# Kernel tuning notes

Hardware: AMD Instinct MI355X
Metric: run time of the kernel (lower is better)

The kernel has to match this reference:

```python
import jax, jax.numpy as jnp
import numpy as np

B, S, XDIM, YDIM = 64, 1024, 256, 128


def setup_inputs() -> dict:
    key = jax.random.key(0)
    ks = jax.random.split(key, 7)
    q = jax.random.normal(ks[0], (B, S, XDIM), dtype=jnp.float32)
    # Linear weights in torch layout [out, in]; biases [out]
    sc = 1.0 / np.sqrt(XDIM)
    Wq = jax.random.normal(ks[1], (YDIM, XDIM), dtype=jnp.float32) * sc
    Wk = jax.random.normal(ks[2], (YDIM, XDIM), dtype=jnp.float32) * sc
    Wv = jax.random.normal(ks[3], (YDIM, XDIM), dtype=jnp.float32) * sc
    bq = jax.random.normal(ks[4], (YDIM,), dtype=jnp.float32) * sc
    bk = jax.random.normal(ks[5], (YDIM,), dtype=jnp.float32) * sc
    bv = jax.random.normal(ks[6], (YDIM,), dtype=jnp.float32) * sc
    return {"q": q, "Wq": Wq, "bq": bq, "Wk": Wk, "bk": bk, "Wv": Wv, "bv": bv}


def reference(q, Wq, bq, Wk, bk, Wv, bv):
    # Q, K, V projections: [B, S, YDIM]
    Q = jnp.einsum('bsx,yx->bsy', q, Wq) + bq
    K = jnp.einsum('bsx,yx->bsy', q, Wk) + bk
    V = jnp.einsum('bsx,yx->bsy', q, Wv) + bv
    scale = jnp.float32(np.sqrt(YDIM))
    # scores [B, S_q, S_k]; softmax over the QUERY axis (dim=-2), non-standard
    scores = jnp.einsum('bqd,bkd->bqk', Q, K) / scale
    attn = jax.nn.softmax(scores, axis=-2)
    out = jnp.einsum('bqk,bkd->bqd', attn, V)  # [B, S, YDIM]
    # flat=True: max over dim=-2 -> [B, YDIM]
    return jnp.max(out, axis=-2)
```

## Files before the change

kernel.cpp:

```cpp
#include <hip/hip_runtime.h>

typedef __bf16 bf16;
typedef __attribute__((ext_vector_type(8))) __bf16 bf16x8;
typedef __attribute__((ext_vector_type(4))) __bf16 bf16x4;
typedef __attribute__((ext_vector_type(4))) float  f32x4;

static __device__ __forceinline__ f32x4 mfma16(bf16x8 a, bf16x8 b, f32x4 c) {
  return __builtin_amdgcn_mfma_f32_16x16x32_bf16(a, b, c, 0, 0, 0);
}
static __device__ __forceinline__ float fexp2(float x) {
  return __builtin_amdgcn_exp2f(x);
}
static __device__ __forceinline__ float flog2(float x) {
  return __builtin_amdgcn_logf(x);
}

#define EXP_C1 (1.4426950408889634f / 11.313708498984760f)

typedef const __attribute__((address_space(1))) unsigned int gas_u32;
typedef __attribute__((address_space(3))) unsigned int las_u32;
#define GLDS16(gp, lp) __builtin_amdgcn_global_load_lds((gas_u32*)(gp), (las_u32*)(lp), 16, 0, 0)

#define WAITN0() __asm__ volatile("s_waitcnt vmcnt(0)" ::: "memory")


__global__ __launch_bounds__(256) void k_prep(
    const float* __restrict__ Wq, const float* __restrict__ Wk,
    const float* __restrict__ Wv, bf16* __restrict__ Wc, float* __restrict__ out)
{
  int id = blockIdx.x * 256 + threadIdx.x;
  if (id < 8192) out[id] = -__builtin_inff();
  int proj = id >> 12, r = id & 4095;
  int g = r >> 7, n = r & 127;
  const float* W = proj == 0 ? Wq : proj == 1 ? Wk : Wv;
  const float sc = (proj == 0) ? EXP_C1 : 1.0f;
  const float4* src = (const float4*)(W + n * 256 + g * 8);
  float4 a = src[0], b = src[1];
  bf16x8 o = { (bf16)(a.x * sc), (bf16)(a.y * sc), (bf16)(a.z * sc), (bf16)(a.w * sc),
               (bf16)(b.x * sc), (bf16)(b.y * sc), (bf16)(b.z * sc), (bf16)(b.w * sc) };
  *(bf16x8*)(Wc + (size_t)proj * 32768 + g * 1024 + n * 8) = o;
}

__global__ __launch_bounds__(256, 4) void k_qkv(
    const float* __restrict__ q, const bf16* __restrict__ Wc,
    const float* __restrict__ bq, const float* __restrict__ bk, const float* __restrict__ bv,
    bf16* __restrict__ Qb, bf16* __restrict__ Kb, bf16* __restrict__ VT)
{
  __shared__ bf16 Al[32 * 520];

  const int tid = threadIdx.x, lane = tid & 63, wave = tid >> 6;
  const int ln = lane & 15, quad = lane >> 4;
  const int wc = wave;
  const int m0 = blockIdx.x * 64;

  {
    const float* src = q + (size_t)m0 * 256;
    for (int it = 0; it < 16; ++it) {
      int f = it * 1024 + tid * 4;
      int r = f >> 8, c = f & 255;
      float4 v = *(const float4*)(src + f);
      bf16x4 o = { (bf16)v.x, (bf16)v.y, (bf16)v.z, (bf16)v.w };
      *(bf16x4*)&Al[(c >> 3) * 520 + r * 8 + (c & 7)] = o;
    }
  }
  __syncthreads();

  const int b = m0 >> 10, st = (m0 & 1023) >> 7, s_off = m0 & 64;
  const size_t tbase = ((size_t)b * 8 + st) * 16384;

  for (int p = 0; p < 3; ++p) {
    const bf16* W = Wc + (size_t)p * 32768;
    const float* bias = p == 0 ? bq : p == 1 ? bk : bv;
    if (p < 2) {
      f32x4 acc[2][4] = {};
      for (int kk = 0; kk < 8; ++kk) {
        int g = kk * 4 + quad;
        bf16x8 ax[4], bw[2];
        for (int t = 0; t < 4; ++t)
          ax[t] = *(const bf16x8*)&Al[g * 520 + (t * 16 + ln) * 8];
        for (int t = 0; t < 2; ++t)
          bw[t] = *(const bf16x8*)(W + g * 1024 + (wc * 32 + t * 16 + ln) * 8);
        for (int i = 0; i < 2; ++i)
          for (int j = 0; j < 4; ++j)
            acc[i][j] = mfma16(bw[i], ax[j], acc[i][j]);
      }
      bf16* dst = (p == 0 ? Qb : Kb) + tbase;
      for (int i = 0; i < 2; ++i) {
        float4 b4 = *(const float4*)&bias[wc * 32 + i * 16 + quad * 4];
        if (p == 0) { b4.x *= EXP_C1; b4.y *= EXP_C1; b4.z *= EXP_C1; b4.w *= EXP_C1; }
        int gd = wc * 4 + i * 2 + (quad >> 1);
        int e0 = (quad & 1) * 4;
        for (int j = 0; j < 4; ++j) {
          int s = s_off + j * 16 + ln;
          bf16x4 o = { (bf16)(acc[i][j][0] + b4.x), (bf16)(acc[i][j][1] + b4.y),
                       (bf16)(acc[i][j][2] + b4.z), (bf16)(acc[i][j][3] + b4.w) };
          *(bf16x4*)&dst[(size_t)gd * 1024 + (size_t)s * 8 + e0] = o;
        }
      }
    } else {
      f32x4 acc[4][2] = {};
      for (int kk = 0; kk < 8; ++kk) {
        int g = kk * 4 + quad;
        bf16x8 ax[4], bw[2];
        for (int t = 0; t < 4; ++t)
          ax[t] = *(const bf16x8*)&Al[g * 520 + (t * 16 + ln) * 8];
        for (int t = 0; t < 2; ++t)
          bw[t] = *(const bf16x8*)(W + g * 1024 + (wc * 32 + t * 16 + ln) * 8);
        for (int i = 0; i < 4; ++i)
          for (int j = 0; j < 2; ++j)
            acc[i][j] = mfma16(ax[i], bw[j], acc[i][j]);
      }
      bf16* dst = VT + tbase;
      for (int j = 0; j < 2; ++j) {
        int d = wc * 32 + j * 16 + ln;
        float bb = bias[d];
        for (int i = 0; i < 4; ++i) {
          int s0 = s_off + i * 16 + quad * 4;
          int G  = (s0 >> 5) * 4 + ((s0 & 15) >> 2);
          int e0 = (s0 & 16) >> 2;
          bf16x4 o = { (bf16)(acc[i][j][0] + bb), (bf16)(acc[i][j][1] + bb),
                       (bf16)(acc[i][j][2] + bb), (bf16)(acc[i][j][3] + bb) };
          *(bf16x4*)&dst[(size_t)G * 1024 + (size_t)d * 8 + e0] = o;
        }
      }
    }
  }
}

__global__ __launch_bounds__(256, 2) void k_stats(
    const bf16* __restrict__ Qb, const bf16* __restrict__ Kb, float* __restrict__ nlg)
{
  __shared__ char Qbuf[2][32768];
  const int b = blockIdx.x, kt = blockIdx.y;
  const int tid = threadIdx.x, lane = tid & 63, wave = tid >> 6;
  const int ln = lane & 15, quad = lane >> 4;

  const bf16* ktile = Kb + ((size_t)b * 8 + kt) * 16384;
  bf16x8 ak[2][4];
  for (int i = 0; i < 2; ++i)
    for (int kk = 0; kk < 4; ++kk)
      ak[i][kk] = *(const bf16x8*)(ktile + (kk * 4 + quad) * 1024 + (wave * 32 + i * 16 + ln) * 8);

  const char* qb_b = (const char*)(Qb + (size_t)b * 8 * 16384);
  for (int c = 0; c < 8; ++c)
    GLDS16(qb_b + (wave * 8 + c) * 1024 + lane * 16, &Qbuf[0][(wave * 8 + c) * 1024]);

  f32x4 csum[2] = {};
  for (int qt = 0; qt < 8; ++qt) {
    WAITN0();
    __syncthreads();
    if (qt < 7)
      for (int c = 0; c < 8; ++c)
        GLDS16(qb_b + (size_t)(qt + 1) * 32768 + (wave * 8 + c) * 1024 + lane * 16,
               &Qbuf[(qt + 1) & 1][(wave * 8 + c) * 1024]);
    const char* Ql = Qbuf[qt & 1];
    for (int jq = 0; jq < 8; ++jq) {
      f32x4 s0 = {}, s1 = {};
      __builtin_amdgcn_s_setprio(1);
      for (int kk = 0; kk < 4; ++kk) {
        bf16x8 bqf = *(const bf16x8*)(Ql + ((kk * 4 + quad) * 2 + (jq >> 2)) * 1024
                                         + ((jq * 16 + ln) & 63) * 16);
        s0 = mfma16(ak[0][kk], bqf, s0);
        s1 = mfma16(ak[1][kk], bqf, s1);
      }
      __builtin_amdgcn_s_setprio(0);
      for (int rr = 0; rr < 4; ++rr) {
        csum[0][rr] += fexp2(s0[rr]);
        csum[1][rr] += fexp2(s1[rr]);
      }
    }
  }
  for (int i = 0; i < 2; ++i)
    for (int rr = 0; rr < 4; ++rr) {
      float v = csum[i][rr];
      v += __shfl_xor(v, 1, 64); v += __shfl_xor(v, 2, 64);
      v += __shfl_xor(v, 4, 64); v += __shfl_xor(v, 8, 64);
      csum[i][rr] = v;
    }
  if (ln == 0) {
    float* dst = nlg + (size_t)b * 1024 + kt * 128 + wave * 32 + quad * 4;
    for (int i = 0; i < 2; ++i)
      for (int rr = 0; rr < 4; ++rr)
        dst[i * 16 + rr] = -flog2(csum[i][rr]);
  }
}

__global__ __launch_bounds__(256, 2) void k_attn(
    const bf16* __restrict__ Qb, const bf16* __restrict__ Kb, const bf16* __restrict__ VT,
    const float* __restrict__ nlg, float* __restrict__ out)
{
  __shared__ char bufK[2][16384];
  __shared__ char bufV[2][16384];
  __shared__ float nll[1024];
  __shared__ float redm[4][128];

  const int b = blockIdx.x, qt = blockIdx.y;
  const int tid = threadIdx.x, lane = tid & 63, wave = tid >> 6;
  const int ln = lane & 15, quad = lane >> 4;

  *(float4*)&nll[tid * 4] = *(const float4*)(nlg + (size_t)b * 1024 + tid * 4);

  const bf16* qtile = Qb + ((size_t)b * 8 + qt) * 16384;
  bf16x8 bq_[2][4];
  for (int j = 0; j < 2; ++j)
    for (int kk = 0; kk < 4; ++kk)
      bq_[j][kk] = *(const bf16x8*)(qtile + (kk * 4 + quad) * 1024 + (wave * 32 + j * 16 + ln) * 8);

  const char* kb_b = (const char*)(Kb + (size_t)b * 8 * 16384);
  const char* vt_b = (const char*)(VT + (size_t)b * 8 * 16384);

#define K_DMA(t) do {                                                            \
    const char* ksrc = kb_b + (size_t)((t) >> 1) * 32768 + ((t) & 1) * 1024;     \
    char* dk = bufK[(t) & 1];                                                    \
    for (int c = 0; c < 4; ++c) {                                                \
      int ch = wave * 4 + c;                                                     \
      GLDS16(ksrc + ch * 2048 + lane * 16, dk + ch * 1024);                      \
    }                                                                            \
  } while (0)
#define V_DMA(t) do {                                                            \
    const char* vsrc = vt_b + (size_t)((t) >> 1) * 32768 + ((t) & 1) * 16384;    \
    char* dv = bufV[(t) & 1];                                                    \
    for (int c = 0; c < 4; ++c) {                                                \
      int ch = wave * 4 + c;                                                     \
      GLDS16(vsrc + (ch >> 1) * 2048 + (ch & 1) * 1024 + lane * 16,              \
             dv + ch * 1024);                                                    \
    }                                                                            \
  } while (0)

#define QK(tt, SN) do {                                                          \
    const char* Kl = bufK[(tt) & 1];                                             \
    _Pragma("unroll")                                                            \
    for (int i = 0; i < 4; ++i) {                                                \
      float4 L4 = *(float4*)&nll[(tt) * 64 + i * 16 + quad * 4];                 \
      f32x4 ini = { L4.x, L4.y, L4.z, L4.w };                                    \
      SN[i][0] = ini; SN[i][1] = ini;                                            \
    }                                                                            \
    __builtin_amdgcn_s_setprio(1);                                               \
    _Pragma("unroll")                                                            \
    for (int kk = 0; kk < 4; ++kk) {                                             \
      bf16x8 ak[4];                                                              \
      _Pragma("unroll")                                                          \
      for (int i = 0; i < 4; ++i)                                                \
        ak[i] = *(const bf16x8*)(Kl + (kk * 4 + quad) * 1024 + (i * 16 + ln) * 16); \
      _Pragma("unroll")                                                          \
      for (int i = 0; i < 4; ++i) {                                              \
        SN[i][0] = mfma16(ak[i], bq_[0][kk], SN[i][0]);                          \
        SN[i][1] = mfma16(ak[i], bq_[1][kk], SN[i][1]);                          \
      }                                                                          \
    }                                                                            \
    __builtin_amdgcn_s_setprio(0);                                               \
  } while (0)

#define EXPPV(tt, SC) do {                                                       \
    const char* Vl = bufV[(tt) & 1];                                             \
    _Pragma("unroll")                                                            \
    for (int s = 0; s < 2; ++s) {                                                \
      f32x4 lo0 = SC[2 * s][0], hi0 = SC[2 * s + 1][0];                          \
      f32x4 lo1 = SC[2 * s][1], hi1 = SC[2 * s + 1][1];                          \
      bf16x8 pf0 = bf16x8{                                                       \
        (bf16)fexp2(lo0[0]), (bf16)fexp2(lo0[1]), (bf16)fexp2(lo0[2]), (bf16)fexp2(lo0[3]), \
        (bf16)fexp2(hi0[0]), (bf16)fexp2(hi0[1]), (bf16)fexp2(hi0[2]), (bf16)fexp2(hi0[3]) }; \
      bf16x8 pf1 = bf16x8{                                                       \
        (bf16)fexp2(lo1[0]), (bf16)fexp2(lo1[1]), (bf16)fexp2(lo1[2]), (bf16)fexp2(lo1[3]), \
        (bf16)fexp2(hi1[0]), (bf16)fexp2(hi1[1]), (bf16)fexp2(hi1[2]), (bf16)fexp2(hi1[3]) }; \
      _Pragma("unroll")                                                          \
      for (int j2 = 0; j2 < 8; ++j2) {                                           \
        bf16x8 bv_ = *(const bf16x8*)(Vl + ((s * 4 + quad) * 2 + (j2 >> 2)) * 1024 \
                                         + ((j2 * 16 + ln) & 63) * 16);          \
        oacc[0][j2] = mfma16(pf0, bv_, oacc[0][j2]);                             \
        oacc[1][j2] = mfma16(pf1, bv_, oacc[1][j2]);                             \
      }                                                                          \
    }                                                                            \
  } while (0)

#define STEP(t, CUR, NXT) do {                                                   \
    WAITN0();                                                                    \
    __syncthreads();                                                             \
    if ((t) < 14) K_DMA((t) + 2);                                                \
    if ((t) < 15) V_DMA((t) + 1);                                                \
    if ((t) < 15) QK((t) + 1, NXT);                                              \
    EXPPV((t), CUR);                                                             \
  } while (0)

  f32x4 oacc[2][8] = {};
  f32x4 sA[4][2], sB[4][2];

  K_DMA(0);
  WAITN0();
  __syncthreads();
  K_DMA(1); V_DMA(0);
  QK(0, sA);

  for (int tp = 0; tp < 8; ++tp) {
    STEP(2 * tp,     sA, sB);
    STEP(2 * tp + 1, sB, sA);
  }
#undef STEP
#undef EXPPV
#undef QK
#undef K_DMA
#undef V_DMA

  for (int j2 = 0; j2 < 8; ++j2) {
    float m = -3.4e38f;
    for (int j = 0; j < 2; ++j)
      for (int rr = 0; rr < 4; ++rr)
        m = fmaxf(m, oacc[j][j2][rr]);
    m = fmaxf(m, __shfl_xor(m, 16, 64));
    m = fmaxf(m, __shfl_xor(m, 32, 64));
    if (lane < 16) redm[wave][j2 * 16 + ln] = m;
  }
  __syncthreads();
  if (tid < 128) {
    float m = fmaxf(fmaxf(redm[0][tid], redm[1][tid]), fmaxf(redm[2][tid], redm[3][tid]));
    float* addr = out + (size_t)b * 128 + tid;
    if (m >= 0.0f) atomicMax((int*)addr, __float_as_int(m));
    else           atomicMin((unsigned int*)addr, __float_as_uint(m));
  }
}

extern "C" void kernel_launch(void* const* d_in, const int* in_sizes, int n_in,
                              void* d_out, int out_size, void* d_ws, size_t ws_size,
                              hipStream_t stream) {
  const float* q  = (const float*)d_in[0];
  const float* Wq = (const float*)d_in[1];
  const float* bq = (const float*)d_in[2];
  const float* Wk = (const float*)d_in[3];
  const float* bk = (const float*)d_in[4];
  const float* Wv = (const float*)d_in[5];
  const float* bv = (const float*)d_in[6];
  float* out = (float*)d_out;

  char* ws = (char*)d_ws;
  bf16*  Qb    = (bf16*)(ws);
  bf16*  Kb    = (bf16*)(ws + (16u << 20));
  bf16*  VT    = (bf16*)(ws + (32u << 20));
  float* nlg   = (float*)(ws + (48u << 20));
  bf16*  Wc    = (bf16*)(ws + (49u << 20));

  k_prep <<<48,           256, 0, stream>>>(Wq, Wk, Wv, Wc, out);
  k_qkv  <<<dim3(1024),   256, 0, stream>>>(q, Wc, bq, bk, bv, Qb, Kb, VT);
  k_stats<<<dim3(64, 8),  256, 0, stream>>>(Qb, Kb, nlg);
  k_attn <<<dim3(64, 8),  256, 0, stream>>>(Qb, Kb, VT, nlg, out);
}
```

Baseline: 86.73 us.

## Make QKV projection persistent with double-buffered async LDS staging of fp32 input

The QKV projection kernel now runs 256 blocks of 512 threads, and each block processes four 64-row tiles in turn. Each next tile is prefetched straight from global memory into a double-buffered, XOR-swizzled LDS buffer using global_load_lds, while the current tile is being computed. The fp32 to bf16 conversion moves to the point where operands are read from LDS. The Q, K and V projections are fused into one k-loop so each input fragment is read once, and MFMA priority is raised. The goal is to hide input load latency and cut the per-block prologue and repeated operand loads, at the cost of 128KB of LDS per block, fewer blocks in flight, and more register pressure.

```diff
diff --git a/kernel.cpp b/kernel.cpp
--- a/kernel.cpp
+++ b/kernel.cpp
@@ -41,90 +41,105 @@
   *(bf16x8*)(Wc + (size_t)proj * 32768 + g * 1024 + n * 8) = o;
 }
 
-__global__ __launch_bounds__(256, 4) void k_qkv(
+__global__ __launch_bounds__(512, 2) void k_qkv(
     const float* __restrict__ q, const bf16* __restrict__ Wc,
     const float* __restrict__ bq, const float* __restrict__ bk, const float* __restrict__ bv,
     bf16* __restrict__ Qb, bf16* __restrict__ Kb, bf16* __restrict__ VT)
 {
-  __shared__ bf16 Al[32 * 520];
+  __shared__ char Alf[2][65536];
 
   const int tid = threadIdx.x, lane = tid & 63, wave = tid >> 6;
   const int ln = lane & 15, quad = lane >> 4;
-  const int wc = wave;
-  const int m0 = blockIdx.x * 64;
-
-  {
-    const float* src = q + (size_t)m0 * 256;
-    for (int it = 0; it < 16; ++it) {
-      int f = it * 1024 + tid * 4;
-      int r = f >> 8, c = f & 255;
-      float4 v = *(const float4*)(src + f);
-      bf16x4 o = { (bf16)v.x, (bf16)v.y, (bf16)v.z, (bf16)v.w };
-      *(bf16x4*)&Al[(c >> 3) * 520 + r * 8 + (c & 7)] = o;
-    }
-  }
-  __syncthreads();
-
-  const int b = m0 >> 10, st = (m0 & 1023) >> 7, s_off = m0 & 64;
-  const size_t tbase = ((size_t)b * 8 + st) * 16384;
-
-  for (int p = 0; p < 3; ++p) {
-    const bf16* W = Wc + (size_t)p * 32768;
-    const float* bias = p == 0 ? bq : p == 1 ? bk : bv;
-    if (p < 2) {
-      f32x4 acc[2][4] = {};
-      for (int kk = 0; kk < 8; ++kk) {
-        int g = kk * 4 + quad;
-        bf16x8 ax[4], bw[2];
-        for (int t = 0; t < 4; ++t)
-          ax[t] = *(const bf16x8*)&Al[g * 520 + (t * 16 + ln) * 8];
-        for (int t = 0; t < 2; ++t)
-          bw[t] = *(const bf16x8*)(W + g * 1024 + (wc * 32 + t * 16 + ln) * 8);
-        for (int i = 0; i < 2; ++i)
-          for (int j = 0; j < 4; ++j)
-            acc[i][j] = mfma16(bw[i], ax[j], acc[i][j]);
-      }
+  const int wr = wave >> 2, wc = wave & 3;
+  const int tile0 = blockIdx.x * 4;
+
+#define STAGE(bi, tile) do {                                                     \
+    const char* src_ = (const char*)(q + (size_t)(tile) * 16384);                \
+    char* d_ = Alf[bi];                                                          \
+    for (int c = 0; c < 8; ++c) {                                                \
+      int ch = wave * 8 + c;                                                     \
+      GLDS16(src_ + ch * 1024 + ((lane * 16) ^ ((ch & 7) << 4)),                 \
+             d_ + ch * 1024);                                                    \
+    }                                                                            \
+  } while (0)
+
+  STAGE(0, tile0);
+
+  for (int it = 0; it < 4; ++it) {
+    WAITN0();
+    __syncthreads();
+    if (it < 3) STAGE((it + 1) & 1, tile0 + it + 1);
+    const char* Bf = Alf[it & 1];
+
+    const int m0 = (tile0 + it) * 64;
+    const int b = m0 >> 10, st = (m0 & 1023) >> 7, s_off = m0 & 64;
+    const size_t tbase = ((size_t)b * 8 + st) * 16384;
+
+    f32x4 aQ[2][2] = {}, aK[2][2] = {}, aV[2][2] = {};
+    for (int kk = 0; kk < 8; ++kk) {
+      int g = kk * 4 + quad;
+      bf16x8 ax[2];
+      for (int t = 0; t < 2; ++t) {
+        int r = wr * 32 + t * 16 + ln;
+        int cb = g * 32, sw = (r & 7) << 4;
+        f32x4 a0 = *(const f32x4*)(Bf + r * 1024 + (cb ^ sw));
+        f32x4 a1 = *(const f32x4*)(Bf + r * 1024 + ((cb + 16) ^ sw));
+        ax[t] = bf16x8{ (bf16)a0[0], (bf16)a0[1], (bf16)a0[2], (bf16)a0[3],
+                        (bf16)a1[0], (bf16)a1[1], (bf16)a1[2], (bf16)a1[3] };
+      }
+      bf16x8 bwQ[2], bwK[2], bwV[2];
+      for (int t2 = 0; t2 < 2; ++t2) {
+        const int off = g * 1024 + (wc * 32 + t2 * 16 + ln) * 8;
+        bwQ[t2] = *(const bf16x8*)(Wc + off);
+        bwK[t2] = *(const bf16x8*)(Wc + 32768 + off);
+        bwV[t2] = *(const bf16x8*)(Wc + 65536 + off);
+      }
+      __builtin_amdgcn_s_setprio(1);
+      for (int i = 0; i < 2; ++i)
+        for (int j = 0; j < 2; ++j) {
+          aQ[i][j] = mfma16(bwQ[i], ax[j], aQ[i][j]);
+          aK[i][j] = mfma16(bwK[i], ax[j], aK[i][j]);
+        }
+      for (int i = 0; i < 2; ++i)
+        for (int j = 0; j < 2; ++j)
+          aV[i][j] = mfma16(ax[i], bwV[j], aV[i][j]);
+      __builtin_amdgcn_s_setprio(0);
+    }
+
+    for (int p = 0; p < 2; ++p) {
       bf16* dst = (p == 0 ? Qb : Kb) + tbase;
+      const float* bias = p == 0 ? bq : bk;
       for (int i = 0; i < 2; ++i) {
         float4 b4 = *(const float4*)&bias[wc * 32 + i * 16 + quad * 4];
         if (p == 0) { b4.x *= EXP_C1; b4.y *= EXP_C1; b4.z *= EXP_C1; b4.w *= EXP_C1; }
         int gd = wc * 4 + i * 2 + (quad >> 1);
         int e0 = (quad & 1) * 4;
-        for (int j = 0; j < 4; ++j) {
-          int s = s_off + j * 16 + ln;
-          bf16x4 o = { (bf16)(acc[i][j][0] + b4.x), (bf16)(acc[i][j][1] + b4.y),
-                       (bf16)(acc[i][j][2] + b4.z), (bf16)(acc[i][j][3] + b4.w) };
+        for (int j = 0; j < 2; ++j) {
+          int s = s_off + wr * 32 + j * 16 + ln;
+          const f32x4 a_ = p == 0 ? aQ[i][j] : aK[i][j];
+          bf16x4 o = { (bf16)(a_[0] + b4.x), (bf16)(a_[1] + b4.y),
+                       (bf16)(a_[2] + b4.z), (bf16)(a_[3] + b4.w) };
           *(bf16x4*)&dst[(size_t)gd * 1024 + (size_t)s * 8 + e0] = o;
         }
       }
-    } else {
-      f32x4 acc[4][2] = {};
-      for (int kk = 0; kk < 8; ++kk) {
-        int g = kk * 4 + quad;
-        bf16x8 ax[4], bw[2];
-        for (int t = 0; t < 4; ++t)
-          ax[t] = *(const bf16x8*)&Al[g * 520 + (t * 16 + ln) * 8];
-        for (int t = 0; t < 2; ++t)
-          bw[t] = *(const bf16x8*)(W + g * 1024 + (wc * 32 + t * 16 + ln) * 8);
-        for (int i = 0; i < 4; ++i)
-          for (int j = 0; j < 2; ++j)
-            acc[i][j] = mfma16(ax[i], bw[j], acc[i][j]);
-      }
+    }
+    {
       bf16* dst = VT + tbase;
       for (int j = 0; j < 2; ++j) {
         int d = wc * 32 + j * 16 + ln;
-        float bb = bias[d];
-        for (int i = 0; i < 4; ++i) {
-          int s0 = s_off + i * 16 + quad * 4;
+        float bb = bv[d];
+        for (int i = 0; i < 2; ++i) {
+          int s0 = s_off + wr * 32 + i * 16 + quad * 4;
           int G  = (s0 >> 5) * 4 + ((s0 & 15) >> 2);
           int e0 = (s0 & 16) >> 2;
-          bf16x4 o = { (bf16)(acc[i][j][0] + bb), (bf16)(acc[i][j][1] + bb),
-                       (bf16)(acc[i][j][2] + bb), (bf16)(acc[i][j][3] + bb) };
+          bf16x4 o = { (bf16)(aV[i][j][0] + bb), (bf16)(aV[i][j][1] + bb),
+                       (bf16)(aV[i][j][2] + bb), (bf16)(aV[i][j][3] + bb) };
           *(bf16x4*)&dst[(size_t)G * 1024 + (size_t)d * 8 + e0] = o;
         }
       }
     }
   }
+#undef STAGE
 }
 
 __global__ __launch_bounds__(256, 2) void k_stats(
@@ -339,7 +354,7 @@
   bf16*  Wc    = (bf16*)(ws + (49u << 20));
 
   k_prep <<<48,           256, 0, stream>>>(Wq, Wk, Wv, Wc, out);
-  k_qkv  <<<dim3(1024),   256, 0, stream>>>(q, Wc, bq, bk, bv, Qb, Kb, VT);
+  k_qkv  <<<dim3(256),    512, 0, stream>>>(q, Wc, bq, bk, bv, Qb, Kb, VT);
   k_stats<<<dim3(64, 8),  256, 0, stream>>>(Qb, Kb, nlg);
   k_attn <<<dim3(64, 8),  256, 0, stream>>>(Qb, Kb, VT, nlg, out);
 }
```

New measurement: 93.68 us. +8.0%, slower.
